# Kernel tuning notes

Measured on AMD Instinct MI355X. Metric: run time of the kernel, lower is better.

The kernel has to match this reference:

```python
import jax, jax.numpy as jnp
import numpy as np

N, E, B, STEPS, THETAS, F, R = 20000, 40000, 32, 32, 64, 3, 1.0


def setup_inputs() -> dict:
    key = jax.random.key(0)
    k1, k2, k3, k4 = jax.random.split(key, 4)
    x = jax.random.normal(k1, (N, F), dtype=jnp.float32)
    v = jax.random.normal(k2, (F, THETAS), dtype=jnp.float32)
    v = v / jnp.linalg.norm(v, axis=0, keepdims=True)  # sphere constraint on directions
    lin = jnp.linspace(-R, R, STEPS, dtype=jnp.float32)
    edge_index = jax.random.randint(k3, (2, E), 0, N, dtype=jnp.int64)
    batch = jnp.sort(jax.random.randint(k4, (N,), 0, B, dtype=jnp.int64))
    return {"x": x, "v": v, "lin": lin, "edge_index": edge_index, "batch": batch}


def _ecc(h, idx, lin, num_segments):
    # h: [M, T] heights; idx: [M] graph ids; lin: [S] thresholds
    # sigmoid(200*(lin - h)) -> [M, S, T], then segment-sum over M -> [B, S, T]
    e = jax.nn.sigmoid(200.0 * (lin[None, :, None] - h[:, None, :]))
    return jax.ops.segment_sum(e, idx, num_segments=num_segments)


def reference(x, v, lin, edge_index, batch):
    nh = x @ v                                            # [N, T] node heights
    eh = jnp.maximum(nh[edge_index[0]], nh[edge_index[1]])  # [E, T] edge heights (max of endpoints)
    edge_batch = batch[edge_index[0]]                     # [E]
    ect_nodes = _ecc(nh, batch, lin, B)                   # [B, S, T]
    ect_edges = _ecc(eh, edge_batch, lin, B)              # [B, S, T]
    return ect_nodes - ect_edges / 2
```

## Files before the change

### kernel.cpp

```cpp
#include <hip/hip_runtime.h>

#define N_NODES 20000
#define N_EDGES 40000
#define NB 32
#define NS 32
#define NT 64
#define NCH 40
#define EPC 1024
#define NPREP 64
#define KBN 8
#define KBE 16
#define STEP200 12.9032258065f
#define WB 0.992f


__global__ __launch_bounds__(256) void prep_kernel(
        const int* __restrict__ ei, const int* __restrict__ batch,
        int* __restrict__ chist, int* __restrict__ node_base,
        float* __restrict__ out_zero) {
    const int t = threadIdx.x;
    const int bid = blockIdx.x;
    for (int idx = bid * 256 + t; idx < NB * NS * NT; idx += NPREP * 256)
        out_zero[idx] = 0.0f;

    if (bid < NCH) {
        __shared__ int h[NB];
        if (t < NB) h[t] = 0;
        __syncthreads();
#pragma unroll
        for (int k = 0; k < 4; k++) {
            const int e = bid * EPC + k * 256 + t;
            if (e < N_EDGES) atomicAdd(&h[batch[ei[e]]], 1);
        }
        __syncthreads();
        if (t < NB) chist[bid * NB + t] = h[t];
    } else if (bid < 60) {
#pragma unroll
        for (int k = 0; k < 4; k++) {
            const int n = (bid - NCH) * 1024 + k * 256 + t;
            if (n < N_NODES) {
                const int bn = batch[n];
                const int bp = (n == 0) ? -1 : batch[n - 1];
                for (int b = bp + 1; b <= bn; b++) node_base[b] = n;
                if (n == N_NODES - 1)
                    for (int b = bn + 1; b <= NB; b++) node_base[b] = N_NODES;
            }
        }
    }
}

__global__ __launch_bounds__(256) void scatter_kernel(
        const int* __restrict__ ei, const int* __restrict__ batch,
        const int* __restrict__ chist, int* __restrict__ ebase_g,
        int2* __restrict__ sedge) {
    __shared__ int cursor[NB];
    __shared__ int base[NB];
    const int t = threadIdx.x;
    if (t < NB) {
        int tot = 0, pre = 0;
#pragma unroll
        for (int c = 0; c < NCH; c++) {
            const int vv = chist[c * NB + t];
            tot += vv;
            if (c < (int)blockIdx.x) pre += vv;
        }
        base[t] = tot;
        cursor[t] = pre;
    }
    __syncthreads();
    if (t == 0) {
        int run = 0;
        for (int b = 0; b < NB; b++) { const int vv = base[b]; base[b] = run; run += vv; }
        if (blockIdx.x == 0) ebase_g[NB] = run;
    }
    __syncthreads();
    if (t < NB) {
        cursor[t] += base[t];
        if (blockIdx.x == 0) ebase_g[t] = base[t];
    }
    __syncthreads();
#pragma unroll
    for (int k = 0; k < 4; k++) {
        const int e = blockIdx.x * EPC + k * 256 + t;
        if (e < N_EDGES) {
            const int s = ei[e];
            const int d = ei[N_EDGES + e];
            const int b = batch[s];
            const int p = atomicAdd(&cursor[b], 1);
            sedge[p] = make_int2(s, d);
        }
    }
}

__global__ __launch_bounds__(256) void ect_main_kernel(
        const float* __restrict__ x, const float* __restrict__ v,
        const int* __restrict__ node_base, const int* __restrict__ ebase,
        const int2* __restrict__ sedge,
        float* __restrict__ out) {
    __shared__ float acc[NS * NT];
    __shared__ int diff[(NS + 1) * NT];
    const int t = threadIdx.x;
#pragma unroll
    for (int j = 0; j < 8; j++) acc[t + 256 * j] = 0.0f;
    for (int idx = t; idx < (NS + 1) * NT; idx += 256) diff[idx] = 0;
    __syncthreads();

    const int lane = t & 63;
    const int wid = __builtin_amdgcn_readfirstlane(t >> 6);
    const bool is_node = blockIdx.x < NB * KBN;
    int b, hi, i0, stride; float w;
    if (is_node) {
        b = blockIdx.x / KBN;
        const int slice = blockIdx.x % KBN;
        const int lo = node_base[b]; hi = node_base[b + 1];
        i0 = lo + slice * 4 + wid; stride = KBN * 4; w = 1.0f;
    } else {
        const int q = blockIdx.x - NB * KBN;
        b = q / KBE;
        const int slice = q % KBE;
        const int lo = ebase[b]; hi = ebase[b + 1];
        i0 = lo + slice * 4 + wid; stride = KBE * 4; w = -0.5f;
    }
    const float v0 = v[lane], v1 = v[NT + lane], v2 = v[2 * NT + lane];

    for (int i = i0; i < hi; i += stride) {
        float h;
        if (is_node) {
            h = fmaf(x[3 * i], v0, fmaf(x[3 * i + 1], v1, x[3 * i + 2] * v2));
        } else {
            const int2 e2 = sedge[i];
            const float hs = fmaf(x[3 * e2.x], v0, fmaf(x[3 * e2.x + 1], v1, x[3 * e2.x + 2] * v2));
            const float hd = fmaf(x[3 * e2.y], v0, fmaf(x[3 * e2.y + 1], v1, x[3 * e2.y + 2] * v2));
            h = fmaxf(hs, hd);
        }
        const float t200h = 200.0f * h;
        const float u = (h + 1.0f) * 15.5f;
        const int kb = (int)ceilf(u - WB);
        const int ke = (int)floorf(u + WB) + 1;
#pragma unroll
        for (int j = 0; j < 2; j++) {
            const int s = kb + j;
            if (s < ke && s >= 0 && s < NS) {
                const float z = fmaf((float)s, STEP200, -200.0f) - t200h;
                const float sig = __builtin_amdgcn_rcpf(1.0f + __expf(-z));
                atomicAdd(&acc[s * NT + lane], sig);
            }
        }
        const int kec = min(max(ke, 0), NS);
        atomicAdd(&diff[kec * NT + lane], 1);
    }
    __syncthreads();

    if (t < NT) {
        int run = 0;
#pragma unroll
        for (int s = 0; s < NS; s++) {
            run += diff[s * NT + t];
            acc[s * NT + t] += (float)run;
        }
    }
    __syncthreads();

    float* ob = out + b * (NS * NT);
#pragma unroll
    for (int j = 0; j < 8; j++) {
        const int idx = t + 256 * j;
        const float val = acc[idx];
        if (val != 0.0f) atomicAdd(&ob[idx], w * val);
    }
}

extern "C" void kernel_launch(void* const* d_in, const int* in_sizes, int n_in,
                              void* d_out, int out_size, void* d_ws, size_t ws_size,
                              hipStream_t stream) {
    const float* x   = (const float*)d_in[0];
    const float* v   = (const float*)d_in[1];
    const int*   ei  = (const int*)d_in[3];
    const int*   bat = (const int*)d_in[4];

    float* out = (float*)d_out;

    int* chist     = (int*)d_ws;
    int* node_base = chist + NCH * NB;
    int* ebase     = node_base + 33;
    int2* sedge    = (int2*)(chist + NCH * NB + 68);

    prep_kernel<<<NPREP, 256, 0, stream>>>(ei, bat, chist, node_base, out);
    scatter_kernel<<<NCH, 256, 0, stream>>>(ei, bat, chist, ebase, sedge);
    ect_main_kernel<<<NB * KBN + NB * KBE, 256, 0, stream>>>(
        x, v, node_base, ebase, sedge, out);
}
```

Measured before the change: 100.5 us.

## Fuse prep, scatter and ECT accumulation into one cooperative kernel

```diff
diff --git a/kernel.cpp b/kernel.cpp
--- a/kernel.cpp
+++ b/kernel.cpp
@@ -1,4 +1,7 @@
 #include <hip/hip_runtime.h>
+#include <hip/hip_cooperative_groups.h>
+
+namespace cg = cooperative_groups;
 
 #define N_NODES 20000
 #define N_EDGES 40000
@@ -7,166 +10,168 @@
 #define NT 64
 #define NCH 40
 #define EPC 1024
-#define NPREP 64
-#define KBN 8
-#define KBE 16
+#define KB 24
+#define NBLK (NB * KB)
+#define NSN 22
 #define STEP200 12.9032258065f
 #define WB 0.992f
 
 
-__global__ __launch_bounds__(256) void prep_kernel(
+__device__ __forceinline__ void accum_item(float h, float w, int lane,
+                                           float* __restrict__ acc,
+                                           float* __restrict__ fdiff) {
+    const float t200h = 200.0f * h;
+    const float u = (h + 1.0f) * 15.5f;
+    const int kb = (int)ceilf(u - WB);
+    const int ke = (int)floorf(u + WB) + 1;
+#pragma unroll
+    for (int j = 0; j < 2; j++) {
+        const int s = kb + j;
+        if (s < ke && s >= 0 && s < NS) {
+            const float z = fmaf((float)s, STEP200, -200.0f) - t200h;
+            const float sig = __builtin_amdgcn_rcpf(1.0f + __expf(-z));
+            atomicAdd(&acc[s * NT + lane], w * sig);
+        }
+    }
+    const int kec = min(max(ke, 0), NS);
+    atomicAdd(&fdiff[kec * NT + lane], w);
+}
+
+__global__ __launch_bounds__(256) void ect_fused(
+        const float* __restrict__ x, const float* __restrict__ v,
         const int* __restrict__ ei, const int* __restrict__ batch,
         int* __restrict__ chist, int* __restrict__ node_base,
-        float* __restrict__ out_zero) {
+        int* __restrict__ ebase, int2* __restrict__ sedge,
+        float* __restrict__ out) {
+    cg::grid_group grid = cg::this_grid();
+
+    __shared__ float acc[NS * NT];
+    __shared__ float fdiff[(NS + 1) * NT];
+    __shared__ int h[NB];
+    __shared__ int base[NB];
+
     const int t = threadIdx.x;
     const int bid = blockIdx.x;
-    for (int idx = bid * 256 + t; idx < NB * NS * NT; idx += NPREP * 256)
-        out_zero[idx] = 0.0f;
+    const int b = bid / KB;
+    const int slot = bid % KB;
+    const int scat = (slot >= NSN) ? (b * 2 + (slot - NSN)) : -1;
 
-    if (bid < NCH) {
-        __shared__ int h[NB];
+#pragma unroll
+    for (int j = 0; j < 8; j++) acc[t + 256 * j] = 0.0f;
+    for (int idx = t; idx < (NS + 1) * NT; idx += 256) fdiff[idx] = 0.0f;
+
+    { const int idx = bid * 256 + t; if (idx < NB * NS * NT) out[idx] = 0.0f; }
+
+    if (scat >= 0 && scat < NCH) {
         if (t < NB) h[t] = 0;
         __syncthreads();
 #pragma unroll
         for (int k = 0; k < 4; k++) {
-            const int e = bid * EPC + k * 256 + t;
+            const int e = scat * EPC + k * 256 + t;
             if (e < N_EDGES) atomicAdd(&h[batch[ei[e]]], 1);
         }
         __syncthreads();
-        if (t < NB) chist[bid * NB + t] = h[t];
-    } else if (bid < 60) {
+        if (t < NB) chist[scat * NB + t] = h[t];
+    } else if (slot == NSN - 1 && b < 20) {
 #pragma unroll
         for (int k = 0; k < 4; k++) {
-            const int n = (bid - NCH) * 1024 + k * 256 + t;
+            const int n = b * 1024 + k * 256 + t;
             if (n < N_NODES) {
                 const int bn = batch[n];
                 const int bp = (n == 0) ? -1 : batch[n - 1];
-                for (int b = bp + 1; b <= bn; b++) node_base[b] = n;
+                for (int q = bp + 1; q <= bn; q++) node_base[q] = n;
                 if (n == N_NODES - 1)
-                    for (int b = bn + 1; b <= NB; b++) node_base[b] = N_NODES;
+                    for (int q = bn + 1; q <= NB; q++) node_base[q] = N_NODES;
             }
         }
     }
-}
 
-__global__ __launch_bounds__(256) void scatter_kernel(
-        const int* __restrict__ ei, const int* __restrict__ batch,
-        const int* __restrict__ chist, int* __restrict__ ebase_g,
-        int2* __restrict__ sedge) {
-    __shared__ int cursor[NB];
-    __shared__ int base[NB];
-    const int t = threadIdx.x;
-    if (t < NB) {
-        int tot = 0, pre = 0;
-#pragma unroll
-        for (int c = 0; c < NCH; c++) {
-            const int vv = chist[c * NB + t];
-            tot += vv;
-            if (c < (int)blockIdx.x) pre += vv;
-        }
-        base[t] = tot;
-        cursor[t] = pre;
-    }
-    __syncthreads();
-    if (t == 0) {
-        int run = 0;
-        for (int b = 0; b < NB; b++) { const int vv = base[b]; base[b] = run; run += vv; }
-        if (blockIdx.x == 0) ebase_g[NB] = run;
-    }
-    __syncthreads();
-    if (t < NB) {
-        cursor[t] += base[t];
-        if (blockIdx.x == 0) ebase_g[t] = base[t];
-    }
-    __syncthreads();
-#pragma unroll
-    for (int k = 0; k < 4; k++) {
-        const int e = blockIdx.x * EPC + k * 256 + t;
-        if (e < N_EDGES) {
-            const int s = ei[e];
-            const int d = ei[N_EDGES + e];
-            const int b = batch[s];
-            const int p = atomicAdd(&cursor[b], 1);
-            sedge[p] = make_int2(s, d);
-        }
-    }
-}
-
-__global__ __launch_bounds__(256) void ect_main_kernel(
-        const float* __restrict__ x, const float* __restrict__ v,
-        const int* __restrict__ node_base, const int* __restrict__ ebase,
-        const int2* __restrict__ sedge,
-        float* __restrict__ out) {
-    __shared__ float acc[NS * NT];
-    __shared__ int diff[(NS + 1) * NT];
-    const int t = threadIdx.x;
-#pragma unroll
-    for (int j = 0; j < 8; j++) acc[t + 256 * j] = 0.0f;
-    for (int idx = t; idx < (NS + 1) * NT; idx += 256) diff[idx] = 0;
-    __syncthreads();
+    grid.sync();
 
     const int lane = t & 63;
     const int wid = __builtin_amdgcn_readfirstlane(t >> 6);
-    const bool is_node = blockIdx.x < NB * KBN;
-    int b, hi, i0, stride; float w;
-    if (is_node) {
-        b = blockIdx.x / KBN;
-        const int slice = blockIdx.x % KBN;
-        const int lo = node_base[b]; hi = node_base[b + 1];
-        i0 = lo + slice * 4 + wid; stride = KBN * 4; w = 1.0f;
-    } else {
-        const int q = blockIdx.x - NB * KBN;
-        b = q / KBE;
-        const int slice = q % KBE;
-        const int lo = ebase[b]; hi = ebase[b + 1];
-        i0 = lo + slice * 4 + wid; stride = KBE * 4; w = -0.5f;
-    }
     const float v0 = v[lane], v1 = v[NT + lane], v2 = v[2 * NT + lane];
 
-    for (int i = i0; i < hi; i += stride) {
-        float h;
-        if (is_node) {
-            h = fmaf(x[3 * i], v0, fmaf(x[3 * i + 1], v1, x[3 * i + 2] * v2));
-        } else {
-            const int2 e2 = sedge[i];
-            const float hs = fmaf(x[3 * e2.x], v0, fmaf(x[3 * e2.x + 1], v1, x[3 * e2.x + 2] * v2));
-            const float hd = fmaf(x[3 * e2.y], v0, fmaf(x[3 * e2.y + 1], v1, x[3 * e2.y + 2] * v2));
-            h = fmaxf(hs, hd);
+    if (scat >= 0 && scat < NCH) {
+        if (t < NB) {
+            int tot = 0, pre = 0;
+#pragma unroll
+            for (int c = 0; c < NCH; c++) {
+                const int vv = chist[c * NB + t];
+                tot += vv;
+                if (c < scat) pre += vv;
+            }
+            base[t] = tot;
+            h[t] = pre;
         }
-        const float t200h = 200.0f * h;
-        const float u = (h + 1.0f) * 15.5f;
-        const int kb = (int)ceilf(u - WB);
-        const int ke = (int)floorf(u + WB) + 1;
+        __syncthreads();
+        if (t == 0) {
+            int run = 0;
+            for (int q = 0; q < NB; q++) { const int vv = base[q]; base[q] = run; run += vv; }
+            if (scat == 0) ebase[NB] = run;
+        }
+        __syncthreads();
+        if (t < NB) {
+            h[t] += base[t];
+            if (scat == 0) ebase[t] = base[t];
+        }
+        __syncthreads();
 #pragma unroll
-        for (int j = 0; j < 2; j++) {
-            const int s = kb + j;
-            if (s < ke && s >= 0 && s < NS) {
-                const float z = fmaf((float)s, STEP200, -200.0f) - t200h;
-                const float sig = __builtin_amdgcn_rcpf(1.0f + __expf(-z));
-                atomicAdd(&acc[s * NT + lane], sig);
+        for (int k = 0; k < 4; k++) {
+            const int e = scat * EPC + k * 256 + t;
+            if (e < N_EDGES) {
+                const int s = ei[e];
+                const int d = ei[N_EDGES + e];
+                const int bb = batch[s];
+                const int p = atomicAdd(&h[bb], 1);
+                sedge[p] = make_int2(s, d);
             }
         }
-        const int kec = min(max(ke, 0), NS);
-        atomicAdd(&diff[kec * NT + lane], 1);
+    } else if (slot < NSN) {
+        const int lo = node_base[b], hi = node_base[b + 1];
+        const int stride = NSN * 4;
+        for (int i = lo + slot * 4 + wid; i < hi; i += stride) {
+            const float hh = fmaf(x[3 * i], v0, fmaf(x[3 * i + 1], v1, x[3 * i + 2] * v2));
+            accum_item(hh, 1.0f, lane, acc, fdiff);
+        }
     }
+
+    grid.sync();
+
+    {
+        const int lo = ebase[b], hi = ebase[b + 1];
+        const int stride = KB * 4;
+        int i = lo + slot * 4 + wid;
+        if (i < hi) {
+            int2 e2 = sedge[i];
+            while (i < hi) {
+                const int inext = i + stride;
+                const int2 cur = e2;
+                if (inext < hi) e2 = sedge[inext];
+                const float hs = fmaf(x[3 * cur.x], v0, fmaf(x[3 * cur.x + 1], v1, x[3 * cur.x + 2] * v2));
+                const float hd = fmaf(x[3 * cur.y], v0, fmaf(x[3 * cur.y + 1], v1, x[3 * cur.y + 2] * v2));
+                accum_item(fmaxf(hs, hd), -0.5f, lane, acc, fdiff);
+                i = inext;
+            }
+        }
+    }
+
     __syncthreads();
-
     if (t < NT) {
-        int run = 0;
+        float run = 0.0f;
 #pragma unroll
         for (int s = 0; s < NS; s++) {
-            run += diff[s * NT + t];
-            acc[s * NT + t] += (float)run;
+            run += fdiff[s * NT + t];
+            acc[s * NT + t] += run;
         }
     }
     __syncthreads();
-
     float* ob = out + b * (NS * NT);
 #pragma unroll
     for (int j = 0; j < 8; j++) {
         const int idx = t + 256 * j;
         const float val = acc[idx];
-        if (val != 0.0f) atomicAdd(&ob[idx], w * val);
+        if (val != 0.0f) atomicAdd(&ob[idx], val);
     }
 }
 
@@ -183,10 +188,11 @@
     int* chist     = (int*)d_ws;
     int* node_base = chist + NCH * NB;
     int* ebase     = node_base + 33;
-    int2* sedge    = (int2*)(chist + NCH * NB + 68);
+    int2* sedge    = (int2*)(chist + 1348);
 
-    prep_kernel<<<NPREP, 256, 0, stream>>>(ei, bat, chist, node_base, out);
-    scatter_kernel<<<NCH, 256, 0, stream>>>(ei, bat, chist, ebase, sedge);
-    ect_main_kernel<<<NB * KBN + NB * KBE, 256, 0, stream>>>(
-        x, v, node_base, ebase, sedge, out);
+    void* args[] = { (void*)&x, (void*)&v, (void*)&ei, (void*)&bat,
+                     (void*)&chist, (void*)&node_base, (void*)&ebase,
+                     (void*)&sedge, (void*)&out };
+    hipLaunchCooperativeKernel((const void*)ect_fused, dim3(NBLK), dim3(256),
+                               args, 0, stream);
 }
```

Measured after the change: 287.6 us. +186.2%, slower.

## Merge edge scatter into prep kernel using fixed-capacity per-graph buckets

Applied to the files above, without the earlier changes.

```diff
diff --git a/kernel.cpp b/kernel.cpp
--- a/kernel.cpp
+++ b/kernel.cpp
@@ -5,9 +5,10 @@
 #define NB 32
 #define NS 32
 #define NT 64
+#define EPC 1024
 #define NCH 40
-#define EPC 1024
 #define NPREP 64
+#define CAP 2048
 #define KBN 8
 #define KBE 16
 #define STEP200 12.9032258065f
@@ -16,8 +17,8 @@
 
 __global__ __launch_bounds__(256) void prep_kernel(
         const int* __restrict__ ei, const int* __restrict__ batch,
-        int* __restrict__ chist, int* __restrict__ node_base,
-        float* __restrict__ out_zero) {
+        int* __restrict__ ecnt, int* __restrict__ node_base,
+        int2* __restrict__ sedge, float* __restrict__ out_zero) {
     const int t = threadIdx.x;
     const int bid = blockIdx.x;
     for (int idx = bid * 256 + t; idx < NB * NS * NT; idx += NPREP * 256)
@@ -25,15 +26,35 @@
 
     if (bid < NCH) {
         __shared__ int h[NB];
+        __shared__ int basep[NB];
+        int bb[4], ss[4], dd[4];
         if (t < NB) h[t] = 0;
         __syncthreads();
 #pragma unroll
         for (int k = 0; k < 4; k++) {
             const int e = bid * EPC + k * 256 + t;
-            if (e < N_EDGES) atomicAdd(&h[batch[ei[e]]], 1);
+            bb[k] = -1;
+            if (e < N_EDGES) {
+                ss[k] = ei[e];
+                dd[k] = ei[N_EDGES + e];
+                bb[k] = batch[ss[k]];
+                atomicAdd(&h[bb[k]], 1);
+            }
         }
         __syncthreads();
-        if (t < NB) chist[bid * NB + t] = h[t];
+        if (t < NB) {
+            basep[t] = atomicAdd(&ecnt[t], h[t]);
+            h[t] = 0;
+        }
+        __syncthreads();
+#pragma unroll
+        for (int k = 0; k < 4; k++) {
+            if (bb[k] >= 0) {
+                const int p = atomicAdd(&h[bb[k]], 1);
+                const int g = basep[bb[k]] + p;
+                if (g < CAP) sedge[bb[k] * CAP + g] = make_int2(ss[k], dd[k]);
+            }
+        }
     } else if (bid < 60) {
 #pragma unroll
         for (int k = 0; k < 4; k++) {
@@ -41,60 +62,17 @@
             if (n < N_NODES) {
                 const int bn = batch[n];
                 const int bp = (n == 0) ? -1 : batch[n - 1];
-                for (int b = bp + 1; b <= bn; b++) node_base[b] = n;
+                for (int q = bp + 1; q <= bn; q++) node_base[q] = n;
                 if (n == N_NODES - 1)
-                    for (int b = bn + 1; b <= NB; b++) node_base[b] = N_NODES;
+                    for (int q = bn + 1; q <= NB; q++) node_base[q] = N_NODES;
             }
-        }
-    }
-}
-
-__global__ __launch_bounds__(256) void scatter_kernel(
-        const int* __restrict__ ei, const int* __restrict__ batch,
-        const int* __restrict__ chist, int* __restrict__ ebase_g,
-        int2* __restrict__ sedge) {
-    __shared__ int cursor[NB];
-    __shared__ int base[NB];
-    const int t = threadIdx.x;
-    if (t < NB) {
-        int tot = 0, pre = 0;
-#pragma unroll
-        for (int c = 0; c < NCH; c++) {
-            const int vv = chist[c * NB + t];
-            tot += vv;
-            if (c < (int)blockIdx.x) pre += vv;
-        }
-        base[t] = tot;
-        cursor[t] = pre;
-    }
-    __syncthreads();
-    if (t == 0) {
-        int run = 0;
-        for (int b = 0; b < NB; b++) { const int vv = base[b]; base[b] = run; run += vv; }
-        if (blockIdx.x == 0) ebase_g[NB] = run;
-    }
-    __syncthreads();
-    if (t < NB) {
-        cursor[t] += base[t];
-        if (blockIdx.x == 0) ebase_g[t] = base[t];
-    }
-    __syncthreads();
-#pragma unroll
-    for (int k = 0; k < 4; k++) {
-        const int e = blockIdx.x * EPC + k * 256 + t;
-        if (e < N_EDGES) {
-            const int s = ei[e];
-            const int d = ei[N_EDGES + e];
-            const int b = batch[s];
-            const int p = atomicAdd(&cursor[b], 1);
-            sedge[p] = make_int2(s, d);
         }
     }
 }
 
 __global__ __launch_bounds__(256) void ect_main_kernel(
         const float* __restrict__ x, const float* __restrict__ v,
-        const int* __restrict__ node_base, const int* __restrict__ ebase,
+        const int* __restrict__ node_base, const int* __restrict__ ecnt,
         const int2* __restrict__ sedge,
         float* __restrict__ out) {
     __shared__ float acc[NS * NT];
@@ -118,36 +96,59 @@
         const int q = blockIdx.x - NB * KBN;
         b = q / KBE;
         const int slice = q % KBE;
-        const int lo = ebase[b]; hi = ebase[b + 1];
+        const int lo = b * CAP; hi = lo + ecnt[b];
         i0 = lo + slice * 4 + wid; stride = KBE * 4; w = -0.5f;
     }
     const float v0 = v[lane], v1 = v[NT + lane], v2 = v[2 * NT + lane];
 
-    for (int i = i0; i < hi; i += stride) {
-        float h;
-        if (is_node) {
-            h = fmaf(x[3 * i], v0, fmaf(x[3 * i + 1], v1, x[3 * i + 2] * v2));
-        } else {
-            const int2 e2 = sedge[i];
-            const float hs = fmaf(x[3 * e2.x], v0, fmaf(x[3 * e2.x + 1], v1, x[3 * e2.x + 2] * v2));
-            const float hd = fmaf(x[3 * e2.y], v0, fmaf(x[3 * e2.y + 1], v1, x[3 * e2.y + 2] * v2));
-            h = fmaxf(hs, hd);
+    if (is_node) {
+        for (int i = i0; i < hi; i += stride) {
+            const float h = fmaf(x[3 * i], v0, fmaf(x[3 * i + 1], v1, x[3 * i + 2] * v2));
+            const float t200h = 200.0f * h;
+            const float u = (h + 1.0f) * 15.5f;
+            const int kb = (int)ceilf(u - WB);
+            const int ke = (int)floorf(u + WB) + 1;
+#pragma unroll
+            for (int j = 0; j < 2; j++) {
+                const int s = kb + j;
+                if (s < ke && s >= 0 && s < NS) {
+                    const float z = fmaf((float)s, STEP200, -200.0f) - t200h;
+                    const float sig = __builtin_amdgcn_rcpf(1.0f + __expf(-z));
+                    atomicAdd(&acc[s * NT + lane], sig);
+                }
+            }
+            const int kec = min(max(ke, 0), NS);
+            atomicAdd(&diff[kec * NT + lane], 1);
         }
-        const float t200h = 200.0f * h;
-        const float u = (h + 1.0f) * 15.5f;
-        const int kb = (int)ceilf(u - WB);
-        const int ke = (int)floorf(u + WB) + 1;
+    } else {
+        int i = i0;
+        if (i < hi) {
+            int2 e2 = sedge[i];
+            while (i < hi) {
+                const int inext = i + stride;
+                const int2 cur = e2;
+                if (inext < hi) e2 = sedge[inext];
+                const float hs = fmaf(x[3 * cur.x], v0, fmaf(x[3 * cur.x + 1], v1, x[3 * cur.x + 2] * v2));
+                const float hd = fmaf(x[3 * cur.y], v0, fmaf(x[3 * cur.y + 1], v1, x[3 * cur.y + 2] * v2));
+                const float h = fmaxf(hs, hd);
+                const float t200h = 200.0f * h;
+                const float u = (h + 1.0f) * 15.5f;
+                const int kb = (int)ceilf(u - WB);
+                const int ke = (int)floorf(u + WB) + 1;
 #pragma unroll
-        for (int j = 0; j < 2; j++) {
-            const int s = kb + j;
-            if (s < ke && s >= 0 && s < NS) {
-                const float z = fmaf((float)s, STEP200, -200.0f) - t200h;
-                const float sig = __builtin_amdgcn_rcpf(1.0f + __expf(-z));
-                atomicAdd(&acc[s * NT + lane], sig);
+                for (int j = 0; j < 2; j++) {
+                    const int s = kb + j;
+                    if (s < ke && s >= 0 && s < NS) {
+                        const float z = fmaf((float)s, STEP200, -200.0f) - t200h;
+                        const float sig = __builtin_amdgcn_rcpf(1.0f + __expf(-z));
+                        atomicAdd(&acc[s * NT + lane], sig);
+                    }
+                }
+                const int kec = min(max(ke, 0), NS);
+                atomicAdd(&diff[kec * NT + lane], 1);
+                i = inext;
             }
         }
-        const int kec = min(max(ke, 0), NS);
-        atomicAdd(&diff[kec * NT + lane], 1);
     }
     __syncthreads();
 
@@ -180,13 +181,12 @@
 
     float* out = (float*)d_out;
 
-    int* chist     = (int*)d_ws;
-    int* node_base = chist + NCH * NB;
-    int* ebase     = node_base + 33;
-    int2* sedge    = (int2*)(chist + NCH * NB + 68);
+    int* ecnt      = (int*)d_ws;
+    int* node_base = ecnt + NB;
+    int2* sedge    = (int2*)((int*)d_ws + 72);
 
-    prep_kernel<<<NPREP, 256, 0, stream>>>(ei, bat, chist, node_base, out);
-    scatter_kernel<<<NCH, 256, 0, stream>>>(ei, bat, chist, ebase, sedge);
-    ect_main_kernel<<<NB * KBN + NB * KBE, 256, 0, stream>>>(
-        x, v, node_base, ebase, sedge, out);
+    hipMemsetAsync(ecnt, 0, NB * sizeof(int), stream);
+    prep_kernel<<<NPREP, 256, 0, stream>>>(ei, bat, ecnt, node_base, sedge, out);
+    ect_main_kernel<<<NB * (KBN + KBE), 256, 0, stream>>>(
+        x, v, node_base, ecnt, sedge, out);
 }
```

Measured after the change: 97.53 us. -2.9%, faster.
